# Performance work log

Measured on AMD Instinct MI355X. Metric: run time of the kernel, lower is better.

## Reference

```python
import jax, jax.numpy as jnp
import numpy as np

IN_C = 256
INTER_C = 128


def _conv1x1(x_flat, w, b):
    # x_flat: [n, c_in, N]; w: [c_out, c_in]; b: [c_out] -> [n, c_out, N]
    return jnp.einsum('oc,bcn->bon', w, x_flat) + b[None, :, None]


def setup_inputs() -> dict:
    key = jax.random.key(0)
    ks = jax.random.split(key, 9)
    x = jax.random.normal(ks[0], (4, IN_C, 64, 64), dtype=jnp.float32)
    s_in = 1.0 / np.sqrt(IN_C)
    s_mid = 1.0 / np.sqrt(INTER_C)
    return {
        'x': x,
        'g_w': jax.random.uniform(ks[1], (INTER_C, IN_C), jnp.float32, -s_in, s_in),
        'g_b': jax.random.uniform(ks[2], (INTER_C,), jnp.float32, -s_in, s_in),
        'theta_w': jax.random.uniform(ks[3], (INTER_C, IN_C), jnp.float32, -s_in, s_in),
        'theta_b': jax.random.uniform(ks[4], (INTER_C,), jnp.float32, -s_in, s_in),
        'phi_w': jax.random.uniform(ks[5], (INTER_C, IN_C), jnp.float32, -s_in, s_in),
        'phi_b': jax.random.uniform(ks[6], (INTER_C,), jnp.float32, -s_in, s_in),
        'out_w': jax.random.uniform(ks[7], (IN_C, INTER_C), jnp.float32, -s_mid, s_mid),
        'out_b': jax.random.uniform(ks[8], (IN_C,), jnp.float32, -s_mid, s_mid),
    }


def reference(x, g_w, g_b, theta_w, theta_b, phi_w, phi_b, out_w, out_b):
    n, c, h, w = x.shape
    N = h * w
    x_flat = x.reshape(n, c, N)
    # 1x1-conv projections
    g_x = _conv1x1(x_flat, g_w, g_b).transpose(0, 2, 1)       # [n, N, ci]
    theta_x = _conv1x1(x_flat, theta_w, theta_b).transpose(0, 2, 1)  # [n, N, ci]
    phi_x = _conv1x1(x_flat, phi_w, phi_b)                    # [n, ci, N]
    # dot_product variant: pairwise weight normalized by N (no softmax)
    pairwise_weight = jnp.matmul(theta_x, phi_x) / N          # [n, N, N]
    y = jnp.matmul(pairwise_weight, g_x)                      # [n, N, ci]
    y = y.transpose(0, 2, 1)                                  # [n, ci, N]
    out = x_flat + _conv1x1(y, out_w, out_b)                  # residual
    return out.reshape(n, c, h, w)
```

## Files before the change

### kernel.cpp

```cpp
#include <hip/hip_runtime.h>
#include <hip/hip_bf16.h>


#define CC   256
#define NSP  4096
#define NB   4
#define KSPLIT 32

typedef __attribute__((ext_vector_type(8))) short bf16x8;
typedef __attribute__((ext_vector_type(4))) float f32x4;

#define F_WEND 2097152
#define H_TT   0
#define H_PG   2097152
#define H_S2   6291456
#define H_WH   6356992
#define H_W2   6455296

__device__ __forceinline__ unsigned short f2bf(float f) {
  __hip_bfloat16 h = __float2bfloat16(f);
  return __builtin_bit_cast(unsigned short, h);
}
__device__ __forceinline__ uint4 pack8(const unsigned short* h) {
  uint4 u;
  u.x = (unsigned)h[0] | ((unsigned)h[1] << 16);
  u.y = (unsigned)h[2] | ((unsigned)h[3] << 16);
  u.z = (unsigned)h[4] | ((unsigned)h[5] << 16);
  u.w = (unsigned)h[6] | ((unsigned)h[7] << 16);
  return u;
}
__device__ __forceinline__ bf16x8 ld_cvt8(const float* __restrict__ p) {
  float4 lo = *(const float4*)p;
  float4 hi = *(const float4*)(p + 4);
  bf16x8 r;
  r[0] = (short)f2bf(lo.x); r[1] = (short)f2bf(lo.y);
  r[2] = (short)f2bf(lo.z); r[3] = (short)f2bf(lo.w);
  r[4] = (short)f2bf(hi.x); r[5] = (short)f2bf(hi.y);
  r[6] = (short)f2bf(hi.z); r[7] = (short)f2bf(hi.w);
  return r;
}

__device__ __forceinline__ void wave_gemm_bt(const unsigned short* __restrict__ A, int pitchA,
                                             const unsigned short* __restrict__ B, int pitchB,
                                             int K, int lane, f32x4 acc[4][4]) {
  int lm = lane & 15, lq = lane >> 4;
  const unsigned short* ap[4];
  const unsigned short* bp[4];
#pragma unroll
  for (int i = 0; i < 4; ++i) {
    ap[i] = A + (size_t)(i * 16 + lm) * pitchA + lq * 8;
    bp[i] = B + (size_t)(i * 16 + lm) * pitchB + lq * 8;
  }
  bf16x8 a0[4], b0[4];
#pragma unroll
  for (int i = 0; i < 4; ++i) {
    a0[i] = *(const bf16x8*)(ap[i]);
    b0[i] = *(const bf16x8*)(bp[i]);
  }
  for (int k = 32; k < K; k += 32) {
    bf16x8 a1[4], b1[4];
#pragma unroll
    for (int i = 0; i < 4; ++i) {
      a1[i] = *(const bf16x8*)(ap[i] + k);
      b1[i] = *(const bf16x8*)(bp[i] + k);
    }
#pragma unroll
    for (int mi = 0; mi < 4; ++mi)
#pragma unroll
      for (int ni = 0; ni < 4; ++ni)
        acc[mi][ni] = __builtin_amdgcn_mfma_f32_16x16x32_bf16(a0[mi], b0[ni], acc[mi][ni], 0, 0, 0);
#pragma unroll
    for (int i = 0; i < 4; ++i) { a0[i] = a1[i]; b0[i] = b1[i]; }
  }
#pragma unroll
  for (int mi = 0; mi < 4; ++mi)
#pragma unroll
    for (int ni = 0; ni < 4; ++ni)
      acc[mi][ni] = __builtin_amdgcn_mfma_f32_16x16x32_bf16(a0[mi], b0[ni], acc[mi][ni], 0, 0, 0);
}

__global__ __launch_bounds__(256) void kW(const float* __restrict__ g_w,
                                          const float* __restrict__ theta_w,
                                          const float* __restrict__ phi_w,
                                          unsigned short* __restrict__ wsh) {
  int idx = (blockIdx.x * 256 + threadIdx.x) * 4;
  int r = idx >> 8;
  const float* src = (r < 128) ? (g_w + idx)
                   : (r < 256) ? (theta_w + idx - 32768)
                               : (phi_w + idx - 65536);
  float4 v = *(const float4*)src;
  uint2 o;
  o.x = (unsigned)f2bf(v.x) | ((unsigned)f2bf(v.y) << 16);
  o.y = (unsigned)f2bf(v.z) | ((unsigned)f2bf(v.w) << 16);
  *(uint2*)(wsh + H_WH + idx) = o;
}

__global__ __launch_bounds__(256) void kP(
    const float* __restrict__ g_b, const float* __restrict__ theta_b,
    const float* __restrict__ phi_b, const float* __restrict__ x,
    unsigned short* __restrict__ wsh) {
  __shared__ float T[64][33];
  __shared__ unsigned short XL[32 * 256];
  __shared__ float biasL[384];
  int bid = blockIdx.x;
  int b = bid >> 7, c = bid & 127;
  int t = threadIdx.x;
  if (t < 128) {
    biasL[t]       = g_b[t];
    biasL[128 + t] = theta_b[t];
    biasL[256 + t] = phi_b[t];
  }
  for (int s = 0; s < 4; ++s) {
    int r = t >> 2, j = t & 3;
    const float* xr = x + ((size_t)b * CC + s * 64 + r) * NSP + c * 32 + j * 8;
    float4 f0 = *(const float4*)(xr);
    float4 f1 = *(const float4*)(xr + 4);
    T[r][j * 8 + 0] = f0.x; T[r][j * 8 + 1] = f0.y;
    T[r][j * 8 + 2] = f0.z; T[r][j * 8 + 3] = f0.w;
    T[r][j * 8 + 4] = f1.x; T[r][j * 8 + 5] = f1.y;
    T[r][j * 8 + 6] = f1.z; T[r][j * 8 + 7] = f1.w;
    __syncthreads();
    int nr = t >> 3, j2 = t & 7;
    unsigned short o[8];
#pragma unroll
    for (int i = 0; i < 8; ++i) o[i] = f2bf(T[j2 * 8 + i][nr]);
    int kidx = s * 64 + j2 * 8;
    int sw = (nr & 7) << 3;
    *(uint4*)(XL + ((nr * 256 + kidx) ^ sw)) = pack8(o);
    __syncthreads();
  }

  int w = t >> 6, lane = t & 63;
  int lm = lane & 15, lq = lane >> 4;
  int bsw = (lm & 7) << 3;
  const unsigned short* aw[2];
  int bidx[2];
#pragma unroll
  for (int i = 0; i < 2; ++i)
    aw[i] = wsh + H_WH + (size_t)(w * 32 + i * 16 + lm) * 256 + lq * 8;
#pragma unroll
  for (int j = 0; j < 2; ++j)
    bidx[j] = (j * 16 + lm) * 256 + lq * 8;

  f32x4 ag[2][2] = {}, at2[2][2] = {}, ap2[2][2] = {};
  bf16x8 bb0[2], xg0[2], xt0[2], xp0[2];
#pragma unroll
  for (int j = 0; j < 2; ++j) bb0[j] = *(const bf16x8*)(XL + (bidx[j] ^ bsw));
#pragma unroll
  for (int i = 0; i < 2; ++i) {
    xg0[i] = *(const bf16x8*)(aw[i]);
    xt0[i] = *(const bf16x8*)(aw[i] + 32768);
    xp0[i] = *(const bf16x8*)(aw[i] + 65536);
  }
  for (int k = 32; k < 256; k += 32) {
    bf16x8 bb1[2], xg1[2], xt1[2], xp1[2];
#pragma unroll
    for (int j = 0; j < 2; ++j) bb1[j] = *(const bf16x8*)(XL + ((bidx[j] + k) ^ bsw));
#pragma unroll
    for (int i = 0; i < 2; ++i) {
      xg1[i] = *(const bf16x8*)(aw[i] + k);
      xt1[i] = *(const bf16x8*)(aw[i] + 32768 + k);
      xp1[i] = *(const bf16x8*)(aw[i] + 65536 + k);
    }
#pragma unroll
    for (int mi = 0; mi < 2; ++mi)
#pragma unroll
      for (int ni = 0; ni < 2; ++ni) {
        ag[mi][ni]  = __builtin_amdgcn_mfma_f32_16x16x32_bf16(xg0[mi], bb0[ni], ag[mi][ni], 0, 0, 0);
        at2[mi][ni] = __builtin_amdgcn_mfma_f32_16x16x32_bf16(xt0[mi], bb0[ni], at2[mi][ni], 0, 0, 0);
        ap2[mi][ni] = __builtin_amdgcn_mfma_f32_16x16x32_bf16(xp0[mi], bb0[ni], ap2[mi][ni], 0, 0, 0);
      }
#pragma unroll
    for (int i = 0; i < 2; ++i) {
      bb0[i] = bb1[i]; xg0[i] = xg1[i]; xt0[i] = xt1[i]; xp0[i] = xp1[i];
    }
  }
#pragma unroll
  for (int mi = 0; mi < 2; ++mi)
#pragma unroll
    for (int ni = 0; ni < 2; ++ni) {
      ag[mi][ni]  = __builtin_amdgcn_mfma_f32_16x16x32_bf16(xg0[mi], bb0[ni], ag[mi][ni], 0, 0, 0);
      at2[mi][ni] = __builtin_amdgcn_mfma_f32_16x16x32_bf16(xt0[mi], bb0[ni], at2[mi][ni], 0, 0, 0);
      ap2[mi][ni] = __builtin_amdgcn_mfma_f32_16x16x32_bf16(xp0[mi], bb0[ni], ap2[mi][ni], 0, 0, 0);
    }

  size_t tb = (size_t)b * 524288;
#pragma unroll
  for (int mi = 0; mi < 2; ++mi) {
    int p0 = w * 32 + mi * 16 + lq * 4;
#pragma unroll
    for (int ni = 0; ni < 2; ++ni) {
      int n = c * 32 + ni * 16 + lm;
      unsigned short u0 = f2bf(at2[mi][ni][0] + biasL[128 + p0 + 0]);
      unsigned short u1 = f2bf(at2[mi][ni][1] + biasL[128 + p0 + 1]);
      unsigned short u2 = f2bf(at2[mi][ni][2] + biasL[128 + p0 + 2]);
      unsigned short u3 = f2bf(at2[mi][ni][3] + biasL[128 + p0 + 3]);
      uint2 o;
      o.x = (unsigned)u0 | ((unsigned)u1 << 16);
      o.y = (unsigned)u2 | ((unsigned)u3 << 16);
      *(uint2*)(wsh + H_TT + tb + (size_t)n * 128 + p0) = o;
    }
  }

  __syncthreads();
#pragma unroll
  for (int mi = 0; mi < 2; ++mi)
#pragma unroll
    for (int ni = 0; ni < 2; ++ni) {
      int nl = ni * 16 + lm;
#pragma unroll
      for (int rr = 0; rr < 4; ++rr) {
        int p = w * 32 + mi * 16 + lq * 4 + rr;
        XL[p * 32 + nl]         = f2bf(ag[mi][ni][rr] + biasL[p]);
        XL[(128 + p) * 32 + nl] = f2bf(ap2[mi][ni][rr] + biasL[256 + p]);
      }
    }
  __syncthreads();
  size_t pbo = (size_t)b * 1048576;
#pragma unroll
  for (int r4 = 0; r4 < 4; ++r4) {
    int row = r4 * 64 + (t >> 2);
    int coff = (t & 3) * 8;
    *(uint4*)(wsh + H_PG + pbo + (size_t)row * NSP + c * 32 + coff) =
        *(uint4*)(XL + row * 32 + coff);
  }
}

__global__ __launch_bounds__(256) void kS(const unsigned short* __restrict__ wsh,
                                          float* __restrict__ wsf) {
  int bid = blockIdx.x;
  int b = bid >> 5, ks = bid & 31;
  int t = threadIdx.x, w = t >> 6, lane = t & 63;
  int lm = lane & 15, lq = lane >> 4;
  int qm = w >> 1, qn = w & 1;
  const unsigned short* A = wsh + H_PG + (size_t)b * 1048576 +
                            (size_t)(128 + qm * 64) * NSP + ks * 128;
  const unsigned short* B = wsh + H_PG + (size_t)b * 1048576 +
                            (size_t)(qn * 64) * NSP + ks * 128;
  f32x4 acc[4][4] = {};
  wave_gemm_bt(A, NSP, B, NSP, 128, lane, acc);
  float* P = wsf + (size_t)(b * KSPLIT + ks) * 16384;
#pragma unroll
  for (int mi = 0; mi < 4; ++mi)
#pragma unroll
    for (int rr = 0; rr < 4; ++rr) {
      int p = qm * 64 + mi * 16 + lq * 4 + rr;
#pragma unroll
      for (int ni = 0; ni < 4; ++ni)
        P[p * 128 + qn * 64 + ni * 16 + lm] = acc[mi][ni][rr];
    }
}

__global__ __launch_bounds__(256) void kR(const float* __restrict__ wsf,
                                          unsigned short* __restrict__ wsh) {
  int bid = blockIdx.x;
  int b = bid >> 4, e = bid & 15;
  int t = threadIdx.x;
  int base = e * 1024 + t * 4;
  const float* PB = wsf + (size_t)b * KSPLIT * 16384;
  float4 s = {0.f, 0.f, 0.f, 0.f};
#pragma unroll
  for (int ks = 0; ks < KSPLIT; ++ks) {
    float4 p = *(const float4*)(PB + (size_t)ks * 16384 + base);
    s.x += p.x; s.y += p.y; s.z += p.z; s.w += p.w;
  }
  uint2 o;
  o.x = (unsigned)f2bf(s.x) | ((unsigned)f2bf(s.y) << 16);
  o.y = (unsigned)f2bf(s.z) | ((unsigned)f2bf(s.w) << 16);
  *(uint2*)(wsh + H_S2 + (size_t)b * 16384 + base) = o;
}

__global__ __launch_bounds__(256) void kW2(unsigned short* __restrict__ wsh,
                                           const float* __restrict__ out_w) {
  int bid = blockIdx.x;
  int b = bid >> 2, is = bid & 3;
  int t = threadIdx.x, w = t >> 6, lane = t & 63;
  int lm = lane & 15, lq = lane >> 4;
  const unsigned short* B = wsh + H_S2 + (size_t)b * 16384 + (size_t)(w * 32) * 128;
  f32x4 acc[4][2] = {};
  for (int k = 0; k < 128; k += 32) {
    bf16x8 a[4], bb[2];
#pragma unroll
    for (int i = 0; i < 4; ++i)
      a[i] = ld_cvt8(out_w + (size_t)(is * 64 + i * 16 + lm) * 128 + lq * 8 + k);
#pragma unroll
    for (int j = 0; j < 2; ++j)
      bb[j] = *(const bf16x8*)(B + (size_t)(j * 16 + lm) * 128 + lq * 8 + k);
#pragma unroll
    for (int mi = 0; mi < 4; ++mi)
#pragma unroll
      for (int ni = 0; ni < 2; ++ni)
        acc[mi][ni] = __builtin_amdgcn_mfma_f32_16x16x32_bf16(a[mi], bb[ni], acc[mi][ni], 0, 0, 0);
  }
  const float inv = 1.0f / 4096.0f;
#pragma unroll
  for (int mi = 0; mi < 4; ++mi)
#pragma unroll
    for (int rr = 0; rr < 4; ++rr) {
      int i = is * 64 + mi * 16 + lq * 4 + rr;
#pragma unroll
      for (int ni = 0; ni < 2; ++ni) {
        int p = w * 32 + ni * 16 + lm;
        wsh[H_W2 + (size_t)b * 32768 + (size_t)i * 128 + p] = f2bf(acc[mi][ni][rr] * inv);
      }
    }
}

__global__ __launch_bounds__(256) void kD(const unsigned short* __restrict__ wsh,
                                          const float* __restrict__ x,
                                          const float* __restrict__ out_b,
                                          float* __restrict__ out) {
  int bid = blockIdx.x;
  int b = bid >> 8, r8 = bid & 255;
  int rq = r8 >> 6, ct = r8 & 63;
  int t = threadIdx.x, w = t >> 6, lane = t & 63;
  int wm = w >> 1, wn = w & 1;
  int lm = lane & 15, lq = lane >> 4;
  int rb = rq * 64 + wm * 32, cb = ct * 64 + wn * 32;
  const unsigned short* A = wsh + H_W2 + (size_t)b * 32768;
  const unsigned short* B = wsh + H_TT + (size_t)b * 524288;
  const unsigned short* ap[2];
  const unsigned short* bp[2];
#pragma unroll
  for (int i = 0; i < 2; ++i) {
    ap[i] = A + (size_t)(rb + i * 16 + lm) * 128 + lq * 8;
    bp[i] = B + (size_t)(cb + i * 16 + lm) * 128 + lq * 8;
  }
  f32x4 acc[2][2] = {};
  bf16x8 a0[2], b0[2];
#pragma unroll
  for (int i = 0; i < 2; ++i) {
    a0[i] = *(const bf16x8*)(ap[i]);
    b0[i] = *(const bf16x8*)(bp[i]);
  }
  for (int k = 32; k < 128; k += 32) {
    bf16x8 a1[2], b1[2];
#pragma unroll
    for (int i = 0; i < 2; ++i) {
      a1[i] = *(const bf16x8*)(ap[i] + k);
      b1[i] = *(const bf16x8*)(bp[i] + k);
    }
#pragma unroll
    for (int mi = 0; mi < 2; ++mi)
#pragma unroll
      for (int ni = 0; ni < 2; ++ni)
        acc[mi][ni] = __builtin_amdgcn_mfma_f32_16x16x32_bf16(a0[mi], b0[ni], acc[mi][ni], 0, 0, 0);
#pragma unroll
    for (int i = 0; i < 2; ++i) { a0[i] = a1[i]; b0[i] = b1[i]; }
  }
#pragma unroll
  for (int mi = 0; mi < 2; ++mi)
#pragma unroll
    for (int ni = 0; ni < 2; ++ni)
      acc[mi][ni] = __builtin_amdgcn_mfma_f32_16x16x32_bf16(a0[mi], b0[ni], acc[mi][ni], 0, 0, 0);

#pragma unroll
  for (int mi = 0; mi < 2; ++mi)
#pragma unroll
    for (int rr = 0; rr < 4; ++rr) {
      int row = rb + mi * 16 + lq * 4 + rr;
      float bi = out_b[row];
#pragma unroll
      for (int ni = 0; ni < 2; ++ni) {
        int col = cb + ni * 16 + lm;
        size_t off = ((size_t)b * CC + row) * NSP + col;
        out[off] = acc[mi][ni][rr] + x[off] + bi;
      }
    }
}

extern "C" void kernel_launch(void* const* d_in, const int* in_sizes, int n_in,
                              void* d_out, int out_size, void* d_ws, size_t ws_size,
                              hipStream_t stream) {
  const float* x       = (const float*)d_in[0];
  const float* g_w     = (const float*)d_in[1];
  const float* g_b     = (const float*)d_in[2];
  const float* theta_w = (const float*)d_in[3];
  const float* theta_b = (const float*)d_in[4];
  const float* phi_w   = (const float*)d_in[5];
  const float* phi_b   = (const float*)d_in[6];
  const float* out_w   = (const float*)d_in[7];
  const float* out_b   = (const float*)d_in[8];
  float* wsf = (float*)d_ws;
  unsigned short* wsh = (unsigned short*)(wsf + F_WEND);
  float* out = (float*)d_out;

  kW<<<dim3(96), dim3(256), 0, stream>>>(g_w, theta_w, phi_w, wsh);
  kP<<<dim3(512), dim3(256), 0, stream>>>(g_b, theta_b, phi_b, x, wsh);
  kS<<<dim3(128), dim3(256), 0, stream>>>(wsh, wsf);
  kR<<<dim3(64), dim3(256), 0, stream>>>(wsf, wsh);
  kW2<<<dim3(16), dim3(256), 0, stream>>>(wsh, out_w);
  kD<<<dim3(1024), dim3(256), 0, stream>>>(wsh, x, out_b, out);
}
```

Before: 126.5 us.

## Fuse six kernel launches into one cooperative kernel with grid syncs

```diff
diff --git a/kernel.cpp b/kernel.cpp
--- a/kernel.cpp
+++ b/kernel.cpp
@@ -1,5 +1,8 @@
 #include <hip/hip_runtime.h>
 #include <hip/hip_bf16.h>
+#include <hip/hip_cooperative_groups.h>
+
+namespace cg = cooperative_groups;
 
 
 #define CC   256
@@ -79,11 +82,11 @@
       acc[mi][ni] = __builtin_amdgcn_mfma_f32_16x16x32_bf16(a0[mi], b0[ni], acc[mi][ni], 0, 0, 0);
 }
 
-__global__ __launch_bounds__(256) void kW(const float* __restrict__ g_w,
-                                          const float* __restrict__ theta_w,
-                                          const float* __restrict__ phi_w,
-                                          unsigned short* __restrict__ wsh) {
-  int idx = (blockIdx.x * 256 + threadIdx.x) * 4;
+
+__device__ __forceinline__ void phaseW(int bid, int t,
+    const float* __restrict__ g_w, const float* __restrict__ theta_w,
+    const float* __restrict__ phi_w, unsigned short* __restrict__ wsh) {
+  int idx = (bid * 256 + t) * 4;
   int r = idx >> 8;
   const float* src = (r < 128) ? (g_w + idx)
                    : (r < 256) ? (theta_w + idx - 32768)
@@ -95,16 +98,12 @@
   *(uint2*)(wsh + H_WH + idx) = o;
 }
 
-__global__ __launch_bounds__(256) void kP(
+__device__ __forceinline__ void phaseP(int bid, int t,
     const float* __restrict__ g_b, const float* __restrict__ theta_b,
     const float* __restrict__ phi_b, const float* __restrict__ x,
-    unsigned short* __restrict__ wsh) {
-  __shared__ float T[64][33];
-  __shared__ unsigned short XL[32 * 256];
-  __shared__ float biasL[384];
-  int bid = blockIdx.x;
+    unsigned short* __restrict__ wsh,
+    float (*T)[33], unsigned short* XL, float* biasL) {
   int b = bid >> 7, c = bid & 127;
-  int t = threadIdx.x;
   if (t < 128) {
     biasL[t]       = g_b[t];
     biasL[128 + t] = theta_b[t];
@@ -226,11 +225,10 @@
   }
 }
 
-__global__ __launch_bounds__(256) void kS(const unsigned short* __restrict__ wsh,
-                                          float* __restrict__ wsf) {
-  int bid = blockIdx.x;
+__device__ __forceinline__ void phaseS(int bid, int t,
+    const unsigned short* __restrict__ wsh, float* __restrict__ wsf) {
   int b = bid >> 5, ks = bid & 31;
-  int t = threadIdx.x, w = t >> 6, lane = t & 63;
+  int w = t >> 6, lane = t & 63;
   int lm = lane & 15, lq = lane >> 4;
   int qm = w >> 1, qn = w & 1;
   const unsigned short* A = wsh + H_PG + (size_t)b * 1048576 +
@@ -251,11 +249,9 @@
     }
 }
 
-__global__ __launch_bounds__(256) void kR(const float* __restrict__ wsf,
-                                          unsigned short* __restrict__ wsh) {
-  int bid = blockIdx.x;
+__device__ __forceinline__ void phaseR(int bid, int t,
+    const float* __restrict__ wsf, unsigned short* __restrict__ wsh) {
   int b = bid >> 4, e = bid & 15;
-  int t = threadIdx.x;
   int base = e * 1024 + t * 4;
   const float* PB = wsf + (size_t)b * KSPLIT * 16384;
   float4 s = {0.f, 0.f, 0.f, 0.f};
@@ -270,11 +266,10 @@
   *(uint2*)(wsh + H_S2 + (size_t)b * 16384 + base) = o;
 }
 
-__global__ __launch_bounds__(256) void kW2(unsigned short* __restrict__ wsh,
-                                           const float* __restrict__ out_w) {
-  int bid = blockIdx.x;
+__device__ __forceinline__ void phaseW2(int bid, int t,
+    unsigned short* __restrict__ wsh, const float* __restrict__ out_w) {
   int b = bid >> 2, is = bid & 3;
-  int t = threadIdx.x, w = t >> 6, lane = t & 63;
+  int w = t >> 6, lane = t & 63;
   int lm = lane & 15, lq = lane >> 4;
   const unsigned short* B = wsh + H_S2 + (size_t)b * 16384 + (size_t)(w * 32) * 128;
   f32x4 acc[4][2] = {};
@@ -306,14 +301,12 @@
     }
 }
 
-__global__ __launch_bounds__(256) void kD(const unsigned short* __restrict__ wsh,
-                                          const float* __restrict__ x,
-                                          const float* __restrict__ out_b,
-                                          float* __restrict__ out) {
-  int bid = blockIdx.x;
-  int b = bid >> 8, r8 = bid & 255;
+__device__ __forceinline__ void phaseD(int vb, int t,
+    const unsigned short* __restrict__ wsh, const float* __restrict__ x,
+    const float* __restrict__ out_b, float* __restrict__ out) {
+  int b = vb >> 8, r8 = vb & 255;
   int rq = r8 >> 6, ct = r8 & 63;
-  int t = threadIdx.x, w = t >> 6, lane = t & 63;
+  int w = t >> 6, lane = t & 63;
   int wm = w >> 1, wn = w & 1;
   int lm = lane & 15, lq = lane >> 4;
   int rb = rq * 64 + wm * 32, cb = ct * 64 + wn * 32;
@@ -367,6 +360,67 @@
         out[off] = acc[mi][ni][rr] + x[off] + bi;
       }
     }
+}
+
+__global__ __launch_bounds__(256, 2) void fused(
+    const float* __restrict__ g_w, const float* __restrict__ theta_w,
+    const float* __restrict__ phi_w, const float* __restrict__ out_w,
+    const float* __restrict__ g_b, const float* __restrict__ theta_b,
+    const float* __restrict__ phi_b, const float* __restrict__ out_b,
+    const float* __restrict__ x, float* __restrict__ wsf,
+    unsigned short* __restrict__ wsh, float* __restrict__ out) {
+  __shared__ float T[64][33];
+  __shared__ unsigned short XL[32 * 256];
+  __shared__ float biasL[384];
+  cg::grid_group grid = cg::this_grid();
+  int bid = blockIdx.x, t = threadIdx.x;
+
+  if (bid < 96) phaseW(bid, t, g_w, theta_w, phi_w, wsh);
+  grid.sync();
+  phaseP(bid, t, g_b, theta_b, phi_b, x, wsh, T, XL, biasL);
+  grid.sync();
+  if (bid < 128) phaseS(bid, t, wsh, wsf);
+  grid.sync();
+  if (bid < 64) phaseR(bid, t, wsf, wsh);
+  grid.sync();
+  if (bid < 16) phaseW2(bid, t, wsh, out_w);
+  grid.sync();
+  phaseD(bid * 2 + 0, t, wsh, x, out_b, out);
+  phaseD(bid * 2 + 1, t, wsh, x, out_b, out);
+}
+
+__global__ __launch_bounds__(256) void kW(const float* __restrict__ g_w,
+                                          const float* __restrict__ theta_w,
+                                          const float* __restrict__ phi_w,
+                                          unsigned short* __restrict__ wsh) {
+  phaseW(blockIdx.x, threadIdx.x, g_w, theta_w, phi_w, wsh);
+}
+__global__ __launch_bounds__(256) void kP(
+    const float* __restrict__ g_b, const float* __restrict__ theta_b,
+    const float* __restrict__ phi_b, const float* __restrict__ x,
+    unsigned short* __restrict__ wsh) {
+  __shared__ float T[64][33];
+  __shared__ unsigned short XL[32 * 256];
+  __shared__ float biasL[384];
+  phaseP(blockIdx.x, threadIdx.x, g_b, theta_b, phi_b, x, wsh, T, XL, biasL);
+}
+__global__ __launch_bounds__(256) void kS(const unsigned short* __restrict__ wsh,
+                                          float* __restrict__ wsf) {
+  phaseS(blockIdx.x, threadIdx.x, wsh, wsf);
+}
+__global__ __launch_bounds__(256) void kR(const float* __restrict__ wsf,
+                                          unsigned short* __restrict__ wsh) {
+  phaseR(blockIdx.x, threadIdx.x, wsf, wsh);
+}
+__global__ __launch_bounds__(256) void kW2(unsigned short* __restrict__ wsh,
+                                           const float* __restrict__ out_w) {
+  phaseW2(blockIdx.x, threadIdx.x, wsh, out_w);
+}
+__global__ __launch_bounds__(256) void kD(const unsigned short* __restrict__ wsh,
+                                          const float* __restrict__ x,
+                                          const float* __restrict__ out_b,
+                                          float* __restrict__ out) {
+  phaseD(blockIdx.x, threadIdx.x, wsh, x, out_b, out);
 }
 
 extern "C" void kernel_launch(void* const* d_in, const int* in_sizes, int n_in,
@@ -385,10 +439,17 @@
   unsigned short* wsh = (unsigned short*)(wsf + F_WEND);
   float* out = (float*)d_out;
 
-  kW<<<dim3(96), dim3(256), 0, stream>>>(g_w, theta_w, phi_w, wsh);
-  kP<<<dim3(512), dim3(256), 0, stream>>>(g_b, theta_b, phi_b, x, wsh);
-  kS<<<dim3(128), dim3(256), 0, stream>>>(wsh, wsf);
-  kR<<<dim3(64), dim3(256), 0, stream>>>(wsf, wsh);
-  kW2<<<dim3(16), dim3(256), 0, stream>>>(wsh, out_w);
-  kD<<<dim3(1024), dim3(256), 0, stream>>>(wsh, x, out_b, out);
-}
+  void* args[] = {(void*)&g_w, (void*)&theta_w, (void*)&phi_w, (void*)&out_w,
+                  (void*)&g_b, (void*)&theta_b, (void*)&phi_b, (void*)&out_b,
+                  (void*)&x, (void*)&wsf, (void*)&wsh, (void*)&out};
+  hipError_t err = hipLaunchCooperativeKernel((const void*)fused, dim3(512), dim3(256),
+                                              args, 0, stream);
+  if (err != hipSuccess) {
+    kW<<<dim3(96), dim3(256), 0, stream>>>(g_w, theta_w, phi_w, wsh);
+    kP<<<dim3(512), dim3(256), 0, stream>>>(g_b, theta_b, phi_b, x, wsh);
+    kS<<<dim3(128), dim3(256), 0, stream>>>(wsh, wsf);
+    kR<<<dim3(64), dim3(256), 0, stream>>>(wsf, wsh);
+    kW2<<<dim3(16), dim3(256), 0, stream>>>(wsh, out_w);
+    kD<<<dim3(1024), dim3(256), 0, stream>>>(wsh, x, out_b, out);
+  }
+}
```

New measurement: 416.8 us. 3.29x slower.
